# Optimization experiments

Hardware: AMD Instinct MI355X
Metric: run time of the kernel (lower is better)

Reference implementation:

```python
import jax, jax.numpy as jnp
import numpy as np

D_MODEL = 1024
N_HEADS = 16
D_K = D_MODEL // N_HEADS
B, T = 4, 2048


def setup_inputs() -> dict:
    key = jax.random.key(0)
    ks = jax.random.split(key, 6)
    scale = 1.0 / np.sqrt(D_MODEL)
    q = jax.random.normal(ks[0], (B, T, D_MODEL), dtype=jnp.float32)
    # causal mask: True = masked / ignored (upper triangle)
    causal = jnp.triu(jnp.ones((T, T), dtype=bool), k=1)
    mask = jnp.broadcast_to(causal, (B, 1, T, T))
    Wq = jax.random.normal(ks[1], (D_MODEL, D_MODEL), dtype=jnp.float32) * scale
    Wk = jax.random.normal(ks[2], (D_MODEL, D_MODEL), dtype=jnp.float32) * scale
    Wv = jax.random.normal(ks[3], (D_MODEL, D_MODEL), dtype=jnp.float32) * scale
    Wo = jax.random.normal(ks[4], (D_MODEL, D_MODEL), dtype=jnp.float32) * scale
    bq = jnp.zeros((D_MODEL,), jnp.float32)
    bk = jnp.zeros((D_MODEL,), jnp.float32)
    bv = jnp.zeros((D_MODEL,), jnp.float32)
    bo = jnp.zeros((D_MODEL,), jnp.float32)
    return {"q": q, "mask": mask, "Wq": Wq, "bq": bq, "Wk": Wk, "bk": bk,
            "Wv": Wv, "bv": bv, "Wo": Wo, "bo": bo}


def reference(q, mask, Wq, bq, Wk, bk, Wv, bv, Wo, bo):
    # Self-attention: k = v = q (module defaults). Weights stored torch-style
    # (out, in): y = x @ W.T + b.
    b, tq, _ = q.shape
    qh = (q @ Wq.T + bq).reshape(b, tq, N_HEADS, D_K).transpose(0, 2, 1, 3)  # (B,H,T,dk)
    kh = (q @ Wk.T + bk).reshape(b, tq, N_HEADS, D_K).transpose(0, 2, 1, 3)
    vh = (q @ Wv.T + bv).reshape(b, tq, N_HEADS, D_K).transpose(0, 2, 1, 3)
    attn = jnp.einsum('bhqd,bhkd->bhqk', qh, kh) / np.sqrt(D_K).astype(np.float32)
    attn = jnp.where(mask, -jnp.inf, attn)
    attn = jax.nn.softmax(attn, axis=-1)
    out = jnp.einsum('bhqk,bhkd->bhqd', attn, vh)
    out = out.transpose(0, 2, 1, 3).reshape(b, tq, D_MODEL)
    return out @ Wo.T + bo
```

## Files before the change

### kernel.cpp

```cpp
#include <hip/hip_runtime.h>
#include <hip/hip_bf16.h>
#include <stdint.h>

#define D_MODEL 1024
#define NH      16
#define DKH     64
#define BATCH   4
#define SEQ     2048
#define MROWS   (BATCH*SEQ)

typedef __hip_bfloat16 bf16;
typedef __attribute__((ext_vector_type(8))) short  bf16x8;
typedef __attribute__((ext_vector_type(4))) short  bf16x4;
typedef __attribute__((ext_vector_type(4))) float  f32x4;
typedef __attribute__((ext_vector_type(2))) unsigned int u32x2;

#define CEXP 0.18033688011112042f

__device__ __forceinline__ bf16 f2bf(float x){ return __float2bfloat16(x); }

__device__ __forceinline__ void gload_lds16(const void* g, void* l) {
  __builtin_amdgcn_global_load_lds(
      (const __attribute__((address_space(1))) unsigned int*)g,
      (__attribute__((address_space(3))) unsigned int*)l, 16, 0, 0);
}

__device__ __forceinline__ unsigned int cvtpk(float lo, float hi) {
  unsigned int r;
  asm("v_cvt_pk_bf16_f32 %0, %1, %2" : "=v"(r) : "v"(lo), "v"(hi));
  return r;
}

__global__ __launch_bounds__(256)
void cvt_all(const float* __restrict__ q,
             const float* __restrict__ w0, const float* __restrict__ w1,
             const float* __restrict__ w2, const float* __restrict__ w3,
             bf16* __restrict__ qdst, bf16* __restrict__ wdst)
{
  const int NQB = (MROWS * D_MODEL) / 1024;
  const int bid = blockIdx.x;
  const float* src;
  bf16* dst;
  int i;
  if (bid < NQB) {
    src = q; dst = qdst;
    i = bid * 1024 + threadIdx.x * 4;
  } else {
    const int b2 = bid - NQB;
    const int w = b2 >> 10;
    src = (w == 0) ? w0 : (w == 1) ? w1 : (w == 2) ? w2 : w3;
    dst = wdst + (size_t)w * (D_MODEL * D_MODEL);
    i = (b2 & 1023) * 1024 + threadIdx.x * 4;
  }
  f32x4 v = *(const f32x4*)&src[i];
  union { bf16 e[4]; bf16x4 v4; } u;
  u.e[0] = f2bf(v[0]); u.e[1] = f2bf(v[1]);
  u.e[2] = f2bf(v[2]); u.e[3] = f2bf(v[3]);
  *(bf16x4*)&dst[i] = u.v4;
}

template <int MODE>
__global__ __launch_bounds__(512, 2)
void gemm8(const bf16* __restrict__ A, const bf16* __restrict__ W,
           const float* __restrict__ b0, const float* __restrict__ b1,
           const float* __restrict__ b2, void* __restrict__ Cbase)
{
  constexpr int K    = D_MODEL;
  constexpr int NT   = K / 64;
  constexpr int SLOT = (128 + 256) * 64;
  __shared__ __align__(16) short ring[3 * SLOT];

  const int tid  = threadIdx.x;
  const int lane = tid & 63;
  const int wave = tid >> 6;
  const int lm   = lane & 15;
  const int quad = lane >> 4;
  const int wm   = (wave >> 2) * 64;
  const int wn   = (wave & 3) * 64;
  const int bm   = blockIdx.x * 128;
  const int bn   = blockIdx.y * 256;

  const int rr    = tid >> 3;
  const int kperm = ((tid & 7) ^ (rr & 7)) * 8;
  const bf16* aS0 = A + (int64_t)(bm + rr) * K + kperm;
  const bf16* aS1 = aS0 + (int64_t)64 * K;
  const bf16* bS0 = W + (int64_t)(bn + rr) * K + kperm;
  const bf16* bS1 = bS0 + (int64_t)64 * K;
  const bf16* bS2 = bS0 + (int64_t)128 * K;
  const bf16* bS3 = bS0 + (int64_t)192 * K;

  f32x4 acc[4][4] = {};

#define STAGE8(T, S)                                                          \
  do {                                                                        \
    const int k0_ = (T) * 64;                                                 \
    short* As_ = &ring[(S) * SLOT];                                           \
    short* Bs_ = As_ + 128 * 64;                                              \
    gload_lds16(aS0 + k0_, &As_[tid * 8]);                                    \
    gload_lds16(aS1 + k0_, &As_[(tid + 512) * 8]);                            \
    gload_lds16(bS0 + k0_, &Bs_[tid * 8]);                                    \
    gload_lds16(bS1 + k0_, &Bs_[(tid + 512) * 8]);                            \
    gload_lds16(bS2 + k0_, &Bs_[(tid + 1024) * 8]);                           \
    gload_lds16(bS3 + k0_, &Bs_[(tid + 1536) * 8]);                           \
  } while (0)

  STAGE8(0, 0);
  STAGE8(1, 1);

#pragma unroll
  for (int t = 0; t < NT; ++t) {
    if (t < NT - 1) asm volatile("s_waitcnt vmcnt(6)" ::: "memory");
    else            asm volatile("s_waitcnt vmcnt(0)" ::: "memory");
    __builtin_amdgcn_s_barrier();
    asm volatile("" ::: "memory");

    const short* As = &ring[(t % 3) * SLOT];
    const short* Bs = As + 128 * 64;
    short* Ad = &ring[((t + 2) % 3) * SLOT];
    short* Bd = Ad + 128 * 64;
    const bool dost = (t + 2 < NT);
    const int k2 = (t + 2) * 64;

#pragma unroll
    for (int kk = 0; kk < 2; ++kk) {
      bf16x8 af[4], bfr[4];
#pragma unroll
      for (int i = 0; i < 4; ++i) {
        const int ra = wm + i * 16 + lm;
        af[i]  = *(const bf16x8*)&As[ra * 64 + (((kk * 4 + quad) ^ (ra & 7))) * 8];
        const int rb = wn + i * 16 + lm;
        bfr[i] = *(const bf16x8*)&Bs[rb * 64 + (((kk * 4 + quad) ^ (rb & 7))) * 8];
      }
      if (dost) {
        if (kk == 0) {
          gload_lds16(aS0 + k2, &Ad[tid * 8]);
          gload_lds16(aS1 + k2, &Ad[(tid + 512) * 8]);
          gload_lds16(bS0 + k2, &Bd[tid * 8]);
        } else {
          gload_lds16(bS1 + k2, &Bd[(tid + 512) * 8]);
          gload_lds16(bS2 + k2, &Bd[(tid + 1024) * 8]);
          gload_lds16(bS3 + k2, &Bd[(tid + 1536) * 8]);
        }
      }
      __builtin_amdgcn_s_barrier();
      asm volatile("s_waitcnt lgkmcnt(0)" ::: "memory");
      __builtin_amdgcn_sched_barrier(0);
      __builtin_amdgcn_s_setprio(1);
#pragma unroll
      for (int i = 0; i < 4; ++i)
#pragma unroll
        for (int j = 0; j < 4; ++j)
          acc[i][j] = __builtin_amdgcn_mfma_f32_16x16x32_bf16(af[i], bfr[j], acc[i][j], 0, 0, 0);
      __builtin_amdgcn_s_setprio(0);
    }
  }
#undef STAGE8

  if constexpr (MODE == 1) {
    float* Cp = (float*)Cbase;
#pragma unroll
    for (int j = 0; j < 4; ++j) {
      const int n = bn + wn + j * 16 + lm;
      const float bv = b0[n];
#pragma unroll
      for (int i = 0; i < 4; ++i)
#pragma unroll
        for (int r = 0; r < 4; ++r) {
          const int m = bm + wm + i * 16 + quad * 4 + r;
          Cp[(int64_t)m * D_MODEL + n] = acc[i][j][r] + bv;
        }
    }
  } else {
    const int proj = bn >> 10;
    const int nl0  = bn & 1023;
    const float* bias = (proj == 0) ? b0 : (proj == 1) ? b1 : b2;
    if (proj == 2) {
      bf16* Vt = (bf16*)Cbase + 2 * (size_t)MROWS * D_MODEL;
#pragma unroll
      for (int j = 0; j < 4; ++j) {
        const int nl = nl0 + wn + j * 16 + lm;
        const float bv = bias[nl];
#pragma unroll
        for (int i = 0; i < 4; ++i) {
          const int m0 = bm + wm + i * 16 + quad * 4;
          const int t0 = m0 & 2047;
          const int j64 = t0 & 63;
          const int pos = (((j64 >> 5) * 4 + ((j64 >> 2) & 3)) << 3)
                        + (((j64 >> 4) & 1) << 2);
          const int64_t base = (int64_t)((m0 >> 11) * 16 + (nl >> 6)) * (DKH * SEQ)
                             + (nl & 63) * SEQ + (t0 & ~63) + pos;
          union { bf16 e[4]; bf16x4 v4; } u;
#pragma unroll
          for (int r = 0; r < 4; ++r) u.e[r] = f2bf(acc[i][j][r] + bv);
          *(bf16x4*)&Vt[base] = u.v4;
        }
      }
    } else {
      bf16* Cp = (bf16*)Cbase + (size_t)proj * MROWS * D_MODEL;
      const float sc = (proj == 0) ? CEXP : 1.0f;
#pragma unroll
      for (int j = 0; j < 4; ++j) {
        const int nl = nl0 + wn + j * 16 + lm;
        const float bv = bias[nl];
#pragma unroll
        for (int i = 0; i < 4; ++i)
#pragma unroll
          for (int r = 0; r < 4; ++r) {
            const int m = bm + wm + i * 16 + quad * 4 + r;
            Cp[(int64_t)m * D_MODEL + nl] = f2bf((acc[i][j][r] + bv) * sc);
          }
      }
    }
  }
}

__global__ __launch_bounds__(256)
void attn_causal(const bf16* __restrict__ Q, const bf16* __restrict__ Kg,
                 const bf16* __restrict__ Vt, bf16* __restrict__ O)
{
  __shared__ __align__(16) short lK[2][64 * 64];
  __shared__ __align__(16) short lV[2][64 * 64];

  const int bid  = blockIdx.x;
  const int qt   = 31 - (bid >> 6);
  const int bh   = bid & 63;

  const int tid  = threadIdx.x;
  const int lane = tid & 63;
  const int wave = tid >> 6;
  const int lm   = lane & 15;
  const int quad = lane >> 4;
  const int qbase = qt * 64;
  const int64_t qkbase = (int64_t)((bh >> 4) * SEQ) * D_MODEL + (bh & 15) * DKH;
  const bf16* Kbase = Kg + qkbase;
  const bf16* Vbase = Vt + (int64_t)bh * DKH * SEQ;

  bf16x8 qf[2];
  {
    const bf16* qrow = Q + qkbase + (int64_t)(qbase + wave * 16 + lm) * D_MODEL;
    qf[0] = *(const bf16x8*)&qrow[quad * 8];
    qf[1] = *(const bf16x8*)&qrow[32 + quad * 8];
  }

  f32x4 o_acc[4] = {};
  f32x4 o_sum   = {};
  const bf16x8 ones8 = {16256, 16256, 16256, 16256,
                        16256, 16256, 16256, 16256};

  const int srow = tid >> 3;
  const int sg   = (tid & 7) ^ (srow & 7);
  const int wqv  = wave * 16 + lm;

  const bf16* kp0 = Kbase + (int64_t)srow        * D_MODEL + sg * 8;
  const bf16* kp1 = Kbase + (int64_t)(srow + 32) * D_MODEL + sg * 8;
  const bf16* vp0 = Vbase + (int64_t)srow        * SEQ + sg * 8;
  const bf16* vp1 = Vbase + (int64_t)(srow + 32) * SEQ + sg * 8;

#define STAGE(KB, BUF)                                                        \
  do {                                                                        \
    gload_lds16(kp0 + (int64_t)(KB) * D_MODEL, &lK[BUF][tid * 8]);            \
    gload_lds16(kp1 + (int64_t)(KB) * D_MODEL, &lK[BUF][(tid + 256) * 8]);    \
    gload_lds16(vp0 + (KB), &lV[BUF][tid * 8]);                               \
    gload_lds16(vp1 + (KB), &lV[BUF][(tid + 256) * 8]);                       \
  } while (0)

  STAGE(0, 0);

  for (int kt = 0; kt <= qt; ++kt) {
    const int cur = kt & 1;
    __syncthreads();
    if (kt < qt) STAGE((kt + 1) * 64, cur ^ 1);

    const short* lKc = lK[cur];
    const short* lVc = lV[cur];

    f32x4 s[4];
    __builtin_amdgcn_s_setprio(1);
#pragma unroll
    for (int ni = 0; ni < 4; ++ni) {
      const int row = ni * 16 + lm;
      f32x4 zz = {};
      bf16x8 k0 = *(const bf16x8*)&lKc[row * 64 + ((quad       ^ (row & 7))) * 8];
      bf16x8 k1 = *(const bf16x8*)&lKc[row * 64 + (((4 + quad) ^ (row & 7))) * 8];
      zz = __builtin_amdgcn_mfma_f32_16x16x32_bf16(k0, qf[0], zz, 0, 0, 0);
      zz = __builtin_amdgcn_mfma_f32_16x16x32_bf16(k1, qf[1], zz, 0, 0, 0);
      s[ni] = zz;
    }
    __builtin_amdgcn_s_setprio(0);

    if (kt == qt) {
#pragma unroll
      for (int ni = 0; ni < 4; ++ni) {
        const int kp = ni * 16 + quad * 4;
#pragma unroll
        for (int r = 0; r < 4; ++r)
          if (kp + r > wqv) s[ni][r] = -1e30f;
      }
    }

    unsigned int pku[4][2];
#pragma unroll
    for (int ni = 0; ni < 4; ++ni) {
      const float p0 = __builtin_amdgcn_exp2f(s[ni][0]);
      const float p1 = __builtin_amdgcn_exp2f(s[ni][1]);
      const float p2 = __builtin_amdgcn_exp2f(s[ni][2]);
      const float p3 = __builtin_amdgcn_exp2f(s[ni][3]);
      pku[ni][0] = cvtpk(p0, p1);
      pku[ni][1] = cvtpk(p2, p3);
    }

    __builtin_amdgcn_s_setprio(1);
#pragma unroll
    for (int m = 0; m < 2; ++m) {
      union { unsigned int u[4]; bf16x8 v; } au;
      au.u[0] = pku[2 * m][0];     au.u[1] = pku[2 * m][1];
      au.u[2] = pku[2 * m + 1][0]; au.u[3] = pku[2 * m + 1][1];
      o_sum = __builtin_amdgcn_mfma_f32_16x16x32_bf16(au.v, ones8, o_sum, 0, 0, 0);
#pragma unroll
      for (int di = 0; di < 4; ++di) {
        const int vrow = di * 16 + lm;
        const bf16x8 vb = *(const bf16x8*)&lVc[vrow * 64
            + (((m * 4 + quad) ^ (vrow & 7))) * 8];
        o_acc[di] = __builtin_amdgcn_mfma_f32_16x16x32_bf16(au.v, vb, o_acc[di], 0, 0, 0);
      }
    }
    __builtin_amdgcn_s_setprio(0);
  }
#undef STAGE

  float lr[4];
#pragma unroll
  for (int r = 0; r < 4; ++r) lr[r] = 1.0f / o_sum[r];

#pragma unroll
  for (int di = 0; di < 4; ++di)
#pragma unroll
    for (int r = 0; r < 4; ++r) {
      const int qrow = qbase + wave * 16 + quad * 4 + r;
      O[qkbase + (int64_t)qrow * D_MODEL + di * 16 + lm] = f2bf(o_acc[di][r] * lr[r]);
    }
}

extern "C" void kernel_launch(void* const* d_in, const int* in_sizes, int n_in,
                              void* d_out, int out_size, void* d_ws, size_t ws_size,
                              hipStream_t stream)
{
  const float* q  = (const float*)d_in[0];
  const float* Wq = (const float*)d_in[2];
  const float* bq = (const float*)d_in[3];
  const float* Wk = (const float*)d_in[4];
  const float* bk = (const float*)d_in[5];
  const float* Wv = (const float*)d_in[6];
  const float* bv = (const float*)d_in[7];
  const float* Wo = (const float*)d_in[8];
  const float* bo = (const float*)d_in[9];
  float* out = (float*)d_out;

  const size_t NQ = (size_t)MROWS * D_MODEL;
  const size_t NW = (size_t)D_MODEL * D_MODEL;

  bf16* qb  = (bf16*)d_ws;
  bf16* Wb  = qb + NQ;
  bf16* Qw  = Wb + 4 * NW;
  bf16* Kw  = Qw + NQ;
  bf16* Vtw = Kw + NQ;

  cvt_all<<<dim3(NQ / 1024 + 4 * NW / 1024), 256, 0, stream>>>(
      q, Wq, Wk, Wv, Wo, qb, Wb);

  gemm8<0><<<dim3(MROWS / 128, 3 * D_MODEL / 256), 512, 0, stream>>>(
      qb, Wb, bq, bk, bv, Qw);

  attn_causal<<<dim3(BATCH * NH * (SEQ / 64)), 256, 0, stream>>>(Qw, Kw, Vtw, qb);

  gemm8<1><<<dim3(MROWS / 128, D_MODEL / 256), 512, 0, stream>>>(
      qb, Wb + 3 * NW, bo, bo, bo, out);
}
```

Measured before the change: 255.4 us.

## Use 256x256-tile double-buffered GEMM for fused QKV projection

```diff
diff --git a/kernel.cpp b/kernel.cpp
--- a/kernel.cpp
+++ b/kernel.cpp
@@ -57,6 +57,148 @@
   u.e[0] = f2bf(v[0]); u.e[1] = f2bf(v[1]);
   u.e[2] = f2bf(v[2]); u.e[3] = f2bf(v[3]);
   *(bf16x4*)&dst[i] = u.v4;
+}
+
+__global__ __launch_bounds__(512, 2)
+void gemm256(const bf16* __restrict__ A, const bf16* __restrict__ W,
+             const float* __restrict__ b0, const float* __restrict__ b1,
+             const float* __restrict__ b2, bf16* __restrict__ Cbase)
+{
+  constexpr int K  = D_MODEL;
+  constexpr int NT = K / 64;
+  constexpr int HS = 256 * 64;
+  __shared__ __align__(16) short lds[2 * 2 * HS];
+
+  const int tid  = threadIdx.x;
+  const int lane = tid & 63;
+  const int wave = tid >> 6;
+  const int lm   = lane & 15;
+  const int quad = lane >> 4;
+  const int wm2  = (wave >> 2) * 128;
+  const int wn2  = (wave & 3) * 64;
+  const int bm   = blockIdx.x * 256;
+  const int bn   = blockIdx.y * 256;
+
+  const int rr    = tid >> 3;
+  const int kperm = ((tid & 7) ^ (rr & 7)) * 8;
+  const bf16* aS = A + (int64_t)(bm + rr) * K + kperm;
+  const bf16* bS = W + (int64_t)(bn + rr) * K + kperm;
+
+  f32x4 acc[8][4] = {};
+
+#define STG_A(S, k0_)                                                         \
+  do { short* d_ = &lds[(S) * 2 * HS];                                        \
+    gload_lds16(aS + (k0_),           &d_[tid * 8]);                          \
+    gload_lds16(aS + (k0_) +  64 * K, &d_[(tid + 512) * 8]);                  \
+    gload_lds16(aS + (k0_) + 128 * K, &d_[(tid + 1024) * 8]);                 \
+    gload_lds16(aS + (k0_) + 192 * K, &d_[(tid + 1536) * 8]); } while (0)
+#define STG_B(S, k0_)                                                         \
+  do { short* d_ = &lds[(S) * 2 * HS + HS];                                   \
+    gload_lds16(bS + (k0_),           &d_[tid * 8]);                          \
+    gload_lds16(bS + (k0_) +  64 * K, &d_[(tid + 512) * 8]);                  \
+    gload_lds16(bS + (k0_) + 128 * K, &d_[(tid + 1024) * 8]);                 \
+    gload_lds16(bS + (k0_) + 192 * K, &d_[(tid + 1536) * 8]); } while (0)
+
+  STG_A(0, 0); STG_B(0, 0);
+  asm volatile("s_waitcnt vmcnt(0)" ::: "memory");
+  __builtin_amdgcn_s_barrier();
+  asm volatile("" ::: "memory");
+
+#define RD_A(kk, mq)                                                          \
+  _Pragma("unroll") for (int i = 0; i < 4; ++i) {                             \
+    const int ra = wm2 + ((mq) * 4 + i) * 16 + lm;                            \
+    af[i] = *(const bf16x8*)&As[ra * 64 + ((((kk) * 4 + quad) ^ (ra & 7))) * 8]; }
+#define RD_B(dst, kk)                                                         \
+  _Pragma("unroll") for (int j = 0; j < 4; ++j) {                             \
+    const int rb = wn2 + j * 16 + lm;                                         \
+    dst[j] = *(const bf16x8*)&Bs[rb * 64 + ((((kk) * 4 + quad) ^ (rb & 7))) * 8]; }
+#define PHASE_SYNC                                                            \
+  __builtin_amdgcn_s_barrier();                                               \
+  asm volatile("s_waitcnt lgkmcnt(0)" ::: "memory");                          \
+  __builtin_amdgcn_sched_barrier(0);
+#define MM(bfv, mq)                                                           \
+  __builtin_amdgcn_s_setprio(1);                                              \
+  _Pragma("unroll") for (int i = 0; i < 4; ++i)                               \
+  _Pragma("unroll") for (int j = 0; j < 4; ++j)                               \
+    acc[(mq) * 4 + i][j] = __builtin_amdgcn_mfma_f32_16x16x32_bf16(          \
+        af[i], bfv[j], acc[(mq) * 4 + i][j], 0, 0, 0);                        \
+  __builtin_amdgcn_s_setprio(0);
+
+#pragma unroll 2
+  for (int t = 0; t < NT; ++t) {
+    const int c = t & 1;
+    const short* As = &lds[c * 2 * HS];
+    const short* Bs = &lds[c * 2 * HS + HS];
+    const bool st = (t + 1 < NT);
+    const int k1 = (t + 1) * 64;
+
+    bf16x8 af[4], bf0[4], bf1[4];
+
+    RD_B(bf0, 0); RD_A(0, 0);
+    if (st) STG_A(c ^ 1, k1);
+    PHASE_SYNC; MM(bf0, 0);
+
+    RD_A(0, 1);
+    if (st) STG_B(c ^ 1, k1);
+    PHASE_SYNC; MM(bf0, 1);
+
+    RD_B(bf1, 1); RD_A(1, 0);
+    PHASE_SYNC; MM(bf1, 0);
+
+    RD_A(1, 1);
+    PHASE_SYNC; MM(bf1, 1);
+
+    asm volatile("s_waitcnt vmcnt(0)" ::: "memory");
+    __builtin_amdgcn_s_barrier();
+    asm volatile("" ::: "memory");
+  }
+#undef STG_A
+#undef STG_B
+#undef RD_A
+#undef RD_B
+#undef PHASE_SYNC
+#undef MM
+
+  const int proj = bn >> 10;
+  const int nl0  = bn & 1023;
+  const float* bias = (proj == 0) ? b0 : (proj == 1) ? b1 : b2;
+  if (proj == 2) {
+    bf16* Vt = Cbase + 2 * (size_t)MROWS * D_MODEL;
+#pragma unroll
+    for (int j = 0; j < 4; ++j) {
+      const int nl = nl0 + wn2 + j * 16 + lm;
+      const float bv = bias[nl];
+#pragma unroll
+      for (int i = 0; i < 8; ++i) {
+        const int m0 = bm + wm2 + i * 16 + quad * 4;
+        const int t0 = m0 & 2047;
+        const int j64 = t0 & 63;
+        const int pos = (((j64 >> 5) * 4 + ((j64 >> 2) & 3)) << 3)
+                      + (((j64 >> 4) & 1) << 2);
+        const int64_t base = (int64_t)((m0 >> 11) * 16 + (nl >> 6)) * (DKH * SEQ)
+                           + (nl & 63) * SEQ + (t0 & ~63) + pos;
+        union { bf16 e[4]; bf16x4 v4; } u;
+#pragma unroll
+        for (int r = 0; r < 4; ++r) u.e[r] = f2bf(acc[i][j][r] + bv);
+        *(bf16x4*)&Vt[base] = u.v4;
+      }
+    }
+  } else {
+    bf16* Cp = Cbase + (size_t)proj * MROWS * D_MODEL;
+    const float sc = (proj == 0) ? CEXP : 1.0f;
+#pragma unroll
+    for (int j = 0; j < 4; ++j) {
+      const int nl = nl0 + wn2 + j * 16 + lm;
+      const float bv = bias[nl];
+#pragma unroll
+      for (int i = 0; i < 8; ++i)
+#pragma unroll
+        for (int r = 0; r < 4; ++r) {
+          const int m = bm + wm2 + i * 16 + quad * 4 + r;
+          Cp[(int64_t)m * D_MODEL + nl] = f2bf((acc[i][j][r] + bv) * sc);
+        }
+    }
+  }
 }
 
 template <int MODE>
@@ -171,45 +313,18 @@
         }
     }
   } else {
-    const int proj = bn >> 10;
-    const int nl0  = bn & 1023;
-    const float* bias = (proj == 0) ? b0 : (proj == 1) ? b1 : b2;
-    if (proj == 2) {
-      bf16* Vt = (bf16*)Cbase + 2 * (size_t)MROWS * D_MODEL;
-#pragma unroll
-      for (int j = 0; j < 4; ++j) {
-        const int nl = nl0 + wn + j * 16 + lm;
-        const float bv = bias[nl];
-#pragma unroll
-        for (int i = 0; i < 4; ++i) {
-          const int m0 = bm + wm + i * 16 + quad * 4;
-          const int t0 = m0 & 2047;
-          const int j64 = t0 & 63;
-          const int pos = (((j64 >> 5) * 4 + ((j64 >> 2) & 3)) << 3)
-                        + (((j64 >> 4) & 1) << 2);
-          const int64_t base = (int64_t)((m0 >> 11) * 16 + (nl >> 6)) * (DKH * SEQ)
-                             + (nl & 63) * SEQ + (t0 & ~63) + pos;
-          union { bf16 e[4]; bf16x4 v4; } u;
-#pragma unroll
-          for (int r = 0; r < 4; ++r) u.e[r] = f2bf(acc[i][j][r] + bv);
-          *(bf16x4*)&Vt[base] = u.v4;
+    bf16* Cp = (bf16*)Cbase;
+#pragma unroll
+    for (int j = 0; j < 4; ++j) {
+      const int n = bn + wn + j * 16 + lm;
+      const float bv = b0[n];
+#pragma unroll
+      for (int i = 0; i < 4; ++i)
+#pragma unroll
+        for (int r = 0; r < 4; ++r) {
+          const int m = bm + wm + i * 16 + quad * 4 + r;
+          Cp[(int64_t)m * D_MODEL + n] = f2bf(acc[i][j][r] + bv);
         }
-      }
-    } else {
-      bf16* Cp = (bf16*)Cbase + (size_t)proj * MROWS * D_MODEL;
-      const float sc = (proj == 0) ? CEXP : 1.0f;
-#pragma unroll
-      for (int j = 0; j < 4; ++j) {
-        const int nl = nl0 + wn + j * 16 + lm;
-        const float bv = bias[nl];
-#pragma unroll
-        for (int i = 0; i < 4; ++i)
-#pragma unroll
-          for (int r = 0; r < 4; ++r) {
-            const int m = bm + wm + i * 16 + quad * 4 + r;
-            Cp[(int64_t)m * D_MODEL + nl] = f2bf((acc[i][j][r] + bv) * sc);
-          }
-      }
     }
   }
 }
@@ -368,7 +483,7 @@
   cvt_all<<<dim3(NQ / 1024 + 4 * NW / 1024), 256, 0, stream>>>(
       q, Wq, Wk, Wv, Wo, qb, Wb);
 
-  gemm8<0><<<dim3(MROWS / 128, 3 * D_MODEL / 256), 512, 0, stream>>>(
+  gemm256<<<dim3(MROWS / 256, 3 * D_MODEL / 256), 512, 0, stream>>>(
       qb, Wb, bq, bk, bv, Qw);
 
   attn_causal<<<dim3(BATCH * NH * (SEQ / 64)), 256, 0, stream>>>(Qw, Kw, Vtw, qb);
```

Measured after the change: 272.4 us. +6.6%, slower.

## Process 128-query tiles per attention block with 8 waves sharing K/V tiles

Applied to the files above, without the earlier changes.

```diff
diff --git a/kernel.cpp b/kernel.cpp
--- a/kernel.cpp
+++ b/kernel.cpp
@@ -214,7 +214,7 @@
   }
 }
 
-__global__ __launch_bounds__(256)
+__global__ __launch_bounds__(512)
 void attn_causal(const bf16* __restrict__ Q, const bf16* __restrict__ Kg,
                  const bf16* __restrict__ Vt, bf16* __restrict__ O)
 {
@@ -222,7 +222,7 @@
   __shared__ __align__(16) short lV[2][64 * 64];
 
   const int bid  = blockIdx.x;
-  const int qt   = 31 - (bid >> 6);
+  const int qt2  = 15 - (bid >> 6);
   const int bh   = bid & 63;
 
   const int tid  = threadIdx.x;
@@ -230,7 +230,8 @@
   const int wave = tid >> 6;
   const int lm   = lane & 15;
   const int quad = lane >> 4;
-  const int qbase = qt * 64;
+  const int qbase = qt2 * 128;
+  const int ktmax = 2 * qt2 + 1;
   const int64_t qkbase = (int64_t)((bh >> 4) * SEQ) * D_MODEL + (bh & 15) * DKH;
   const bf16* Kbase = Kg + qkbase;
   const bf16* Vbase = Vt + (int64_t)bh * DKH * SEQ;
@@ -249,27 +250,24 @@
 
   const int srow = tid >> 3;
   const int sg   = (tid & 7) ^ (srow & 7);
-  const int wqv  = wave * 16 + lm;
-
-  const bf16* kp0 = Kbase + (int64_t)srow        * D_MODEL + sg * 8;
-  const bf16* kp1 = Kbase + (int64_t)(srow + 32) * D_MODEL + sg * 8;
-  const bf16* vp0 = Vbase + (int64_t)srow        * SEQ + sg * 8;
-  const bf16* vp1 = Vbase + (int64_t)(srow + 32) * SEQ + sg * 8;
+  const int wqv  = qbase + wave * 16 + lm;
+  const int wqmin = qbase + wave * 16;
+
+  const bf16* kp = Kbase + (int64_t)srow * D_MODEL + sg * 8;
+  const bf16* vp = Vbase + (int64_t)srow * SEQ + sg * 8;
 
 #define STAGE(KB, BUF)                                                        \
   do {                                                                        \
-    gload_lds16(kp0 + (int64_t)(KB) * D_MODEL, &lK[BUF][tid * 8]);            \
-    gload_lds16(kp1 + (int64_t)(KB) * D_MODEL, &lK[BUF][(tid + 256) * 8]);    \
-    gload_lds16(vp0 + (KB), &lV[BUF][tid * 8]);                               \
-    gload_lds16(vp1 + (KB), &lV[BUF][(tid + 256) * 8]);                       \
+    gload_lds16(kp + (int64_t)(KB) * D_MODEL, &lK[BUF][tid * 8]);             \
+    gload_lds16(vp + (KB), &lV[BUF][tid * 8]);                                \
   } while (0)
 
   STAGE(0, 0);
 
-  for (int kt = 0; kt <= qt; ++kt) {
+  for (int kt = 0; kt <= ktmax; ++kt) {
     const int cur = kt & 1;
     __syncthreads();
-    if (kt < qt) STAGE((kt + 1) * 64, cur ^ 1);
+    if (kt < ktmax) STAGE((kt + 1) * 64, cur ^ 1);
 
     const short* lKc = lK[cur];
     const short* lVc = lV[cur];
@@ -288,13 +286,14 @@
     }
     __builtin_amdgcn_s_setprio(0);
 
-    if (kt == qt) {
+    if (kt * 64 + 63 > wqmin) {
+      const int kb = kt * 64;
 #pragma unroll
       for (int ni = 0; ni < 4; ++ni) {
-        const int kp = ni * 16 + quad * 4;
+        const int kp_ = kb + ni * 16 + quad * 4;
 #pragma unroll
         for (int r = 0; r < 4; ++r)
-          if (kp + r > wqv) s[ni][r] = -1e30f;
+          if (kp_ + r > wqv) s[ni][r] = -1e30f;
       }
     }
 
@@ -371,7 +370,7 @@
   gemm8<0><<<dim3(MROWS / 128, 3 * D_MODEL / 256), 512, 0, stream>>>(
       qb, Wb, bq, bk, bv, Qw);
 
-  attn_causal<<<dim3(BATCH * NH * (SEQ / 64)), 256, 0, stream>>>(Qw, Kw, Vtw, qb);
+  attn_causal<<<dim3(BATCH * NH * (SEQ / 128)), 512, 0, stream>>>(Qw, Kw, Vtw, qb);
 
   gemm8<1><<<dim3(MROWS / 128, D_MODEL / 256), 512, 0, stream>>>(
       qb, Wb + 3 * NW, bo, bo, bo, out);
```

Result: no change. 256.2 us (+0.3%).

## Process two 64-row query tiles per attention block to reuse K/V tiles

Applied to the files above, without the earlier changes.

```diff
diff --git a/kernel.cpp b/kernel.cpp
--- a/kernel.cpp
+++ b/kernel.cpp
@@ -222,7 +222,7 @@
   __shared__ __align__(16) short lV[2][64 * 64];
 
   const int bid  = blockIdx.x;
-  const int qt   = 31 - (bid >> 6);
+  const int qt2  = 15 - (bid >> 6);
   const int bh   = bid & 63;
 
   const int tid  = threadIdx.x;
@@ -230,26 +230,28 @@
   const int wave = tid >> 6;
   const int lm   = lane & 15;
   const int quad = lane >> 4;
-  const int qbase = qt * 64;
+  const int qbase = qt2 * 128;
+  const int ktmax = 2 * qt2 + 1;
   const int64_t qkbase = (int64_t)((bh >> 4) * SEQ) * D_MODEL + (bh & 15) * DKH;
   const bf16* Kbase = Kg + qkbase;
   const bf16* Vbase = Vt + (int64_t)bh * DKH * SEQ;
 
-  bf16x8 qf[2];
-  {
-    const bf16* qrow = Q + qkbase + (int64_t)(qbase + wave * 16 + lm) * D_MODEL;
-    qf[0] = *(const bf16x8*)&qrow[quad * 8];
-    qf[1] = *(const bf16x8*)&qrow[32 + quad * 8];
-  }
-
-  f32x4 o_acc[4] = {};
-  f32x4 o_sum   = {};
+  bf16x8 qf[2][2];
+#pragma unroll
+  for (int g = 0; g < 2; ++g) {
+    const bf16* qrow = Q + qkbase
+        + (int64_t)(qbase + g * 64 + wave * 16 + lm) * D_MODEL;
+    qf[g][0] = *(const bf16x8*)&qrow[quad * 8];
+    qf[g][1] = *(const bf16x8*)&qrow[32 + quad * 8];
+  }
+
+  f32x4 o_acc[2][4] = {};
+  f32x4 o_sum[2]   = {};
   const bf16x8 ones8 = {16256, 16256, 16256, 16256,
                         16256, 16256, 16256, 16256};
 
   const int srow = tid >> 3;
   const int sg   = (tid & 7) ^ (srow & 7);
-  const int wqv  = wave * 16 + lm;
 
   const bf16* kp0 = Kbase + (int64_t)srow        * D_MODEL + sg * 8;
   const bf16* kp1 = Kbase + (int64_t)(srow + 32) * D_MODEL + sg * 8;
@@ -266,79 +268,95 @@
 
   STAGE(0, 0);
 
-  for (int kt = 0; kt <= qt; ++kt) {
+  for (int kt = 0; kt <= ktmax; ++kt) {
     const int cur = kt & 1;
     __syncthreads();
-    if (kt < qt) STAGE((kt + 1) * 64, cur ^ 1);
+    if (kt < ktmax) STAGE((kt + 1) * 64, cur ^ 1);
 
     const short* lKc = lK[cur];
     const short* lVc = lV[cur];
 
-    f32x4 s[4];
+    f32x4 s[2][4];
     __builtin_amdgcn_s_setprio(1);
 #pragma unroll
     for (int ni = 0; ni < 4; ++ni) {
       const int row = ni * 16 + lm;
-      f32x4 zz = {};
-      bf16x8 k0 = *(const bf16x8*)&lKc[row * 64 + ((quad       ^ (row & 7))) * 8];
-      bf16x8 k1 = *(const bf16x8*)&lKc[row * 64 + (((4 + quad) ^ (row & 7))) * 8];
-      zz = __builtin_amdgcn_mfma_f32_16x16x32_bf16(k0, qf[0], zz, 0, 0, 0);
-      zz = __builtin_amdgcn_mfma_f32_16x16x32_bf16(k1, qf[1], zz, 0, 0, 0);
-      s[ni] = zz;
+      const bf16x8 k0 = *(const bf16x8*)&lKc[row * 64 + ((quad       ^ (row & 7))) * 8];
+      const bf16x8 k1 = *(const bf16x8*)&lKc[row * 64 + (((4 + quad) ^ (row & 7))) * 8];
+#pragma unroll
+      for (int g = 0; g < 2; ++g) {
+        f32x4 zz = {};
+        zz = __builtin_amdgcn_mfma_f32_16x16x32_bf16(k0, qf[g][0], zz, 0, 0, 0);
+        zz = __builtin_amdgcn_mfma_f32_16x16x32_bf16(k1, qf[g][1], zz, 0, 0, 0);
+        s[g][ni] = zz;
+      }
     }
     __builtin_amdgcn_s_setprio(0);
 
-    if (kt == qt) {
+#pragma unroll
+    for (int g = 0; g < 2; ++g) {
+      if (kt >= 2 * qt2 + g) {
+        const int qv = qbase + g * 64 + wave * 16 + lm;
+        const int kb = kt * 64;
+#pragma unroll
+        for (int ni = 0; ni < 4; ++ni) {
+          const int kp_ = kb + ni * 16 + quad * 4;
+#pragma unroll
+          for (int r = 0; r < 4; ++r)
+            if (kp_ + r > qv) s[g][ni][r] = -1e30f;
+        }
+      }
+    }
+
+    unsigned int pku[2][4][2];
+#pragma unroll
+    for (int g = 0; g < 2; ++g)
 #pragma unroll
       for (int ni = 0; ni < 4; ++ni) {
-        const int kp = ni * 16 + quad * 4;
-#pragma unroll
-        for (int r = 0; r < 4; ++r)
-          if (kp + r > wqv) s[ni][r] = -1e30f;
-      }
-    }
-
-    unsigned int pku[4][2];
-#pragma unroll
-    for (int ni = 0; ni < 4; ++ni) {
-      const float p0 = __builtin_amdgcn_exp2f(s[ni][0]);
-      const float p1 = __builtin_amdgcn_exp2f(s[ni][1]);
-      const float p2 = __builtin_amdgcn_exp2f(s[ni][2]);
-      const float p3 = __builtin_amdgcn_exp2f(s[ni][3]);
-      pku[ni][0] = cvtpk(p0, p1);
-      pku[ni][1] = cvtpk(p2, p3);
-    }
+        pku[g][ni][0] = cvtpk(__builtin_amdgcn_exp2f(s[g][ni][0]),
+                              __builtin_amdgcn_exp2f(s[g][ni][1]));
+        pku[g][ni][1] = cvtpk(__builtin_amdgcn_exp2f(s[g][ni][2]),
+                              __builtin_amdgcn_exp2f(s[g][ni][3]));
+      }
 
     __builtin_amdgcn_s_setprio(1);
 #pragma unroll
     for (int m = 0; m < 2; ++m) {
-      union { unsigned int u[4]; bf16x8 v; } au;
-      au.u[0] = pku[2 * m][0];     au.u[1] = pku[2 * m][1];
-      au.u[2] = pku[2 * m + 1][0]; au.u[3] = pku[2 * m + 1][1];
-      o_sum = __builtin_amdgcn_mfma_f32_16x16x32_bf16(au.v, ones8, o_sum, 0, 0, 0);
+      union { unsigned int u[4]; bf16x8 v; } au[2];
+#pragma unroll
+      for (int g = 0; g < 2; ++g) {
+        au[g].u[0] = pku[g][2 * m][0];     au[g].u[1] = pku[g][2 * m][1];
+        au[g].u[2] = pku[g][2 * m + 1][0]; au[g].u[3] = pku[g][2 * m + 1][1];
+        o_sum[g] = __builtin_amdgcn_mfma_f32_16x16x32_bf16(au[g].v, ones8, o_sum[g], 0, 0, 0);
+      }
 #pragma unroll
       for (int di = 0; di < 4; ++di) {
         const int vrow = di * 16 + lm;
         const bf16x8 vb = *(const bf16x8*)&lVc[vrow * 64
             + (((m * 4 + quad) ^ (vrow & 7))) * 8];
-        o_acc[di] = __builtin_amdgcn_mfma_f32_16x16x32_bf16(au.v, vb, o_acc[di], 0, 0, 0);
+#pragma unroll
+        for (int g = 0; g < 2; ++g)
+          o_acc[g][di] = __builtin_amdgcn_mfma_f32_16x16x32_bf16(au[g].v, vb, o_acc[g][di], 0, 0, 0);
       }
     }
     __builtin_amdgcn_s_setprio(0);
   }
 #undef STAGE
 
-  float lr[4];
-#pragma unroll
-  for (int r = 0; r < 4; ++r) lr[r] = 1.0f / o_sum[r];
-
-#pragma unroll
-  for (int di = 0; di < 4; ++di)
-#pragma unroll
-    for (int r = 0; r < 4; ++r) {
-      const int qrow = qbase + wave * 16 + quad * 4 + r;
-      O[qkbase + (int64_t)qrow * D_MODEL + di * 16 + lm] = f2bf(o_acc[di][r] * lr[r]);
-    }
+#pragma unroll
+  for (int g = 0; g < 2; ++g) {
+    float lr[4];
+#pragma unroll
+    for (int r = 0; r < 4; ++r) lr[r] = 1.0f / o_sum[g][r];
+#pragma unroll
+    for (int di = 0; di < 4; ++di)
+#pragma unroll
+      for (int r = 0; r < 4; ++r) {
+        const int qrow = qbase + g * 64 + wave * 16 + quad * 4 + r;
+        O[qkbase + (int64_t)qrow * D_MODEL + di * 16 + lm]
+            = f2bf(o_acc[g][di][r] * lr[r]);
+      }
+  }
 }
 
 extern "C" void kernel_launch(void* const* d_in, const int* in_sizes, int n_in,
@@ -371,7 +389,7 @@
   gemm8<0><<<dim3(MROWS / 128, 3 * D_MODEL / 256), 512, 0, stream>>>(
       qb, Wb, bq, bk, bv, Qw);
 
-  attn_causal<<<dim3(BATCH * NH * (SEQ / 64)), 256, 0, stream>>>(Qw, Kw, Vtw, qb);
+  attn_causal<<<dim3(BATCH * NH * (SEQ / 128)), 256, 0, stream>>>(Qw, Kw, Vtw, qb);
 
   gemm8<1><<<dim3(MROWS / 128, D_MODEL / 256), 512, 0, stream>>>(
       qb, Wb + 3 * NW, bo, bo, bo, out);
```

New measurement: 277.2 us. 1.09x slower.
